# Optimization experiments

Hardware: AMD Instinct MI355X
Metric: run time of the kernel (lower is better)

Reference implementation:

```python
import jax, jax.numpy as jnp
import numpy as np

L, P, S, B, W, M = 8, 8, 128, 16, 768, 64


def setup_inputs() -> dict:
    key = jax.random.key(0)
    k0, k1, k2, k3 = jax.random.split(key, 4)
    embeds = jax.random.normal(k0, (L, P, S, B, W), dtype=jnp.float32)
    mask = jax.random.uniform(k1, (B, L, M), dtype=jnp.float32)
    w0 = jax.random.normal(k2, (1, W), dtype=jnp.float32) * 0.02  # dense_0.weight
    b0 = jnp.zeros((1,), dtype=jnp.float32)                       # dense_0.bias
    w1 = jax.random.normal(k3, (1, S), dtype=jnp.float32) * 0.02  # dense_1.weight
    b1 = jnp.zeros((1,), dtype=jnp.float32)                       # dense_1.bias
    return {"embeds": embeds, "mask": mask, "w0": w0, "b0": b0, "w1": w1, "b1": b1}


def reference(embeds, mask, w0, b0, w1, b1):
    # embeds: [L, P, S, B, W]; mask: [B, L, M]
    # dense_0: Linear(W,1) -> scalar per (l,p,s,b)
    x = jnp.einsum('lpsbw,w->lpsb', embeds, w0[0]) + b0[0]
    # dense_1: Linear(S,1) -> scalar per (l,p,b)
    score = jnp.einsum('lpsb,s->lpb', x, w1[0]) + b1[0]
    # sigmoid then softmax over the P (example) axis, per (l,b)
    score = jax.nn.softmax(jax.nn.sigmoid(score), axis=1)  # [L, P, B]
    # max-pool over sequence dim S
    mp = jnp.max(embeds, axis=2)                            # [L, P, B, W]
    # softmax-weighted pooled embeddings, summed over P (the sum over dim=2 in torch)
    sem_sum = jnp.sum(mp * score[..., None], axis=1)        # [L, B, W]
    # tile + mask-multiply + double-sum collapses to a contraction over L
    return jnp.einsum('blm,lbw->bmw', mask, sem_sum)        # [B, M, W]
```

## Files before the change

kernel.cpp:

```cpp
#include <hip/hip_runtime.h>
#include <math.h>

#define L 8
#define P 8
#define S 128
#define B 16
#define W 768
#define M 64

#define LPB (L * P * B)
#define W4 (W / 4)

__global__ __launch_bounds__(W4) void k1_pass(
    const float* __restrict__ embeds,
    const float* __restrict__ w1,
    const float* __restrict__ w0,
    float* __restrict__ mp_out,
    float* __restrict__ score_raw)
{
    const int blk = blockIdx.x;
    const int t   = threadIdx.x;
    const int lp  = blk / B;
    const int b   = blk % B;

    __shared__ float lw1[S];
    if (t < S) lw1[t] = w1[t];
    __syncthreads();

    const float* base = embeds + (size_t)lp * S * B * W + (size_t)b * W + 4 * t;

    float4 acc = make_float4(0.f, 0.f, 0.f, 0.f);
    float4 mp  = make_float4(-INFINITY, -INFINITY, -INFINITY, -INFINITY);

#pragma unroll 8
    for (int s = 0; s < S; ++s) {
        const float4 v = *reinterpret_cast<const float4*>(base + (size_t)s * B * W);
        const float c = lw1[s];
        acc.x = fmaf(c, v.x, acc.x);
        acc.y = fmaf(c, v.y, acc.y);
        acc.z = fmaf(c, v.z, acc.z);
        acc.w = fmaf(c, v.w, acc.w);
        mp.x = fmaxf(mp.x, v.x);
        mp.y = fmaxf(mp.y, v.y);
        mp.z = fmaxf(mp.z, v.z);
        mp.w = fmaxf(mp.w, v.w);
    }

    *reinterpret_cast<float4*>(mp_out + (size_t)blk * W + 4 * t) = mp;

    const float4 w0v = *reinterpret_cast<const float4*>(w0 + 4 * t);
    float part = w0v.x * acc.x + w0v.y * acc.y + w0v.z * acc.z + w0v.w * acc.w;

#pragma unroll
    for (int off = 32; off > 0; off >>= 1)
        part += __shfl_down(part, off, 64);

    __shared__ float wred[3];
    if ((t & 63) == 0) wred[t >> 6] = part;
    __syncthreads();
    if (t == 0) score_raw[blk] = wred[0] + wred[1] + wred[2];
}

__global__ __launch_bounds__(128) void k2_softmax(
    const float* __restrict__ score_raw,
    const float* __restrict__ w1,
    const float* __restrict__ b0,
    const float* __restrict__ b1,
    float* __restrict__ score)
{
    const int idx = threadIdx.x;
    const int l = idx / B;
    const int b = idx % B;

    float sw1 = 0.f;
#pragma unroll
    for (int s = 0; s < S; ++s) sw1 += w1[s];
    const float bias = b0[0] * sw1 + b1[0];

    float sc[P];
    float mx = -INFINITY;
#pragma unroll
    for (int p = 0; p < P; ++p) {
        const float raw = score_raw[(l * P + p) * B + b] + bias;
        sc[p] = 1.f / (1.f + expf(-raw));
        mx = fmaxf(mx, sc[p]);
    }
    float sum = 0.f;
#pragma unroll
    for (int p = 0; p < P; ++p) {
        sc[p] = expf(sc[p] - mx);
        sum += sc[p];
    }
    const float inv = 1.f / sum;
#pragma unroll
    for (int p = 0; p < P; ++p)
        score[(l * P + p) * B + b] = sc[p] * inv;
}

__global__ __launch_bounds__(256) void k3_weighted_sum(
    const float* __restrict__ mp,
    const float* __restrict__ score,
    float* __restrict__ sem)
{
    const int idx = blockIdx.x * 256 + threadIdx.x;
    if (idx >= L * B * W) return;
    const int w  = idx % W;
    const int lb = idx / W;
    const int l  = lb / B;
    const int b  = lb % B;

    float acc = 0.f;
#pragma unroll
    for (int p = 0; p < P; ++p) {
        const int lpb = (l * P + p) * B + b;
        acc = fmaf(score[lpb], mp[(size_t)lpb * W + w], acc);
    }
    sem[(size_t)(l * B + b) * W + w] = acc;
}

__global__ __launch_bounds__(256) void k4_mask_contract(
    const float* __restrict__ mask,
    const float* __restrict__ sem,
    float* __restrict__ out)
{
    const int idx = blockIdx.x * 256 + threadIdx.x;
    if (idx >= B * M * W) return;
    const int w  = idx % W;
    const int bm = idx / W;
    const int m  = bm % M;
    const int b  = bm / M;

    float acc = 0.f;
#pragma unroll
    for (int l = 0; l < L; ++l)
        acc = fmaf(mask[(b * L + l) * M + m], sem[(size_t)(l * B + b) * W + w], acc);
    out[idx] = acc;
}

extern "C" void kernel_launch(void* const* d_in, const int* in_sizes, int n_in,
                              void* d_out, int out_size, void* d_ws, size_t ws_size,
                              hipStream_t stream) {
    const float* embeds = (const float*)d_in[0];
    const float* mask   = (const float*)d_in[1];
    const float* w0     = (const float*)d_in[2];
    const float* b0     = (const float*)d_in[3];
    const float* w1     = (const float*)d_in[4];
    const float* b1     = (const float*)d_in[5];
    float* out = (float*)d_out;

    float* ws        = (float*)d_ws;
    float* mp        = ws;
    float* score_raw = mp + (size_t)LPB * W;
    float* score     = score_raw + LPB;
    float* sem       = score + LPB;

    k1_pass<<<LPB, W4, 0, stream>>>(embeds, w1, w0, mp, score_raw);
    k2_softmax<<<1, 128, 0, stream>>>(score_raw, w1, b0, b1, score);
    k3_weighted_sum<<<(L * B * W + 255) / 256, 256, 0, stream>>>(mp, score, sem);
    k4_mask_contract<<<(B * M * W + 255) / 256, 256, 0, stream>>>(mask, sem, out);
}
```

Measured before the change: 535.3 us.

## Split the sequence reduction across four blocks per (l,p,b) to raise parallelism

The main streaming pass now divides the S axis into four shards, launching four times as many blocks. Each block writes a partial max-pool row and a partial score. The softmax and weighted-sum kernels then combine the shards with a sum and a max. This targets the low block count (1024 blocks of 192 threads) that limits memory-level parallelism when streaming 400MB of embeddings. In exchange, it writes and reads four times as much intermediate max-pool data.

New measurement: 531.6 us. Within noise of the previous version (-0.7%).

```diff
diff --git a/kernel.cpp b/kernel.cpp
--- a/kernel.cpp
+++ b/kernel.cpp
@@ -10,30 +10,36 @@
 
 #define LPB (L * P * B)
 #define W4 (W / 4)
+#define NSH 4
+#define SH (S / NSH)
 
 __global__ __launch_bounds__(W4) void k1_pass(
     const float* __restrict__ embeds,
     const float* __restrict__ w1,
     const float* __restrict__ w0,
-    float* __restrict__ mp_out,
-    float* __restrict__ score_raw)
+    float* __restrict__ mp_part,
+    float* __restrict__ score_part)
 {
-    const int blk = blockIdx.x;
+    const int bid = blockIdx.x;
+    const int sh  = bid / LPB;
+    const int lpb = bid % LPB;
     const int t   = threadIdx.x;
-    const int lp  = blk / B;
-    const int b   = blk % B;
+    const int lp  = lpb / B;
+    const int b   = lpb % B;
 
-    __shared__ float lw1[S];
-    if (t < S) lw1[t] = w1[t];
+    __shared__ float lw1[SH];
+    if (t < SH) lw1[t] = w1[sh * SH + t];
     __syncthreads();
 
-    const float* base = embeds + (size_t)lp * S * B * W + (size_t)b * W + 4 * t;
+    const float* base = embeds + (size_t)lp * S * B * W
+                               + (size_t)(sh * SH) * B * W
+                               + (size_t)b * W + 4 * t;
 
     float4 acc = make_float4(0.f, 0.f, 0.f, 0.f);
     float4 mp  = make_float4(-INFINITY, -INFINITY, -INFINITY, -INFINITY);
 
 #pragma unroll 8
-    for (int s = 0; s < S; ++s) {
+    for (int s = 0; s < SH; ++s) {
         const float4 v = *reinterpret_cast<const float4*>(base + (size_t)s * B * W);
         const float c = lw1[s];
         acc.x = fmaf(c, v.x, acc.x);
@@ -46,7 +52,7 @@
         mp.w = fmaxf(mp.w, v.w);
     }
 
-    *reinterpret_cast<float4*>(mp_out + (size_t)blk * W + 4 * t) = mp;
+    *reinterpret_cast<float4*>(mp_part + ((size_t)sh * LPB + lpb) * W + 4 * t) = mp;
 
     const float4 w0v = *reinterpret_cast<const float4*>(w0 + 4 * t);
     float part = w0v.x * acc.x + w0v.y * acc.y + w0v.z * acc.z + w0v.w * acc.w;
@@ -58,11 +64,11 @@
     __shared__ float wred[3];
     if ((t & 63) == 0) wred[t >> 6] = part;
     __syncthreads();
-    if (t == 0) score_raw[blk] = wred[0] + wred[1] + wred[2];
+    if (t == 0) score_part[(size_t)sh * LPB + lpb] = wred[0] + wred[1] + wred[2];
 }
 
 __global__ __launch_bounds__(128) void k2_softmax(
-    const float* __restrict__ score_raw,
+    const float* __restrict__ score_part,
     const float* __restrict__ w1,
     const float* __restrict__ b0,
     const float* __restrict__ b1,
@@ -81,7 +87,10 @@
     float mx = -INFINITY;
 #pragma unroll
     for (int p = 0; p < P; ++p) {
-        const float raw = score_raw[(l * P + p) * B + b] + bias;
+        const int lpb = (l * P + p) * B + b;
+        float raw = bias;
+#pragma unroll
+        for (int sh = 0; sh < NSH; ++sh) raw += score_part[sh * LPB + lpb];
         sc[p] = 1.f / (1.f + expf(-raw));
         mx = fmaxf(mx, sc[p]);
     }
@@ -98,7 +107,7 @@
 }
 
 __global__ __launch_bounds__(256) void k3_weighted_sum(
-    const float* __restrict__ mp,
+    const float* __restrict__ mp_part,
     const float* __restrict__ score,
     float* __restrict__ sem)
 {
@@ -113,7 +122,11 @@
 #pragma unroll
     for (int p = 0; p < P; ++p) {
         const int lpb = (l * P + p) * B + b;
-        acc = fmaf(score[lpb], mp[(size_t)lpb * W + w], acc);
+        float mp = -INFINITY;
+#pragma unroll
+        for (int sh = 0; sh < NSH; ++sh)
+            mp = fmaxf(mp, mp_part[((size_t)sh * LPB + lpb) * W + w]);
+        acc = fmaf(score[lpb], mp, acc);
     }
     sem[(size_t)(l * B + b) * W + w] = acc;
 }
@@ -148,14 +161,14 @@
     const float* b1     = (const float*)d_in[5];
     float* out = (float*)d_out;
 
-    float* ws        = (float*)d_ws;
-    float* mp        = ws;
-    float* score_raw = mp + (size_t)LPB * W;
-    float* score     = score_raw + LPB;
-    float* sem       = score + LPB;
+    float* ws         = (float*)d_ws;
+    float* mp_part    = ws;
+    float* score_part = mp_part + (size_t)NSH * LPB * W;
+    float* score      = score_part + (size_t)NSH * LPB;
+    float* sem        = score + LPB;
 
-    k1_pass<<<LPB, W4, 0, stream>>>(embeds, w1, w0, mp, score_raw);
-    k2_softmax<<<1, 128, 0, stream>>>(score_raw, w1, b0, b1, score);
-    k3_weighted_sum<<<(L * B * W + 255) / 256, 256, 0, stream>>>(mp, score, sem);
+    k1_pass<<<NSH * LPB, W4, 0, stream>>>(embeds, w1, w0, mp_part, score_part);
+    k2_softmax<<<1, 128, 0, stream>>>(score_part, w1, b0, b1, score);
+    k3_weighted_sum<<<(L * B * W + 255) / 256, 256, 0, stream>>>(mp_part, score, sem);
     k4_mask_contract<<<(B * M * W + 255) / 256, 256, 0, stream>>>(mask, sem, out);
 }
```
